# Optimization experiments

Measured on AMD Instinct MI355X. Metric: run time of the kernel, lower is better.

## Reference

```python
import jax, jax.numpy as jnp
import numpy as np

B, C, H, W = 8, 512, 96, 96
C8 = C // 8


def conv1x1(x, w, b):
    # x: (B,Cin,H,W), w: (Cout,Cin), b: (Cout,)
    return jnp.einsum('bchw,oc->bohw', x, w) + b[None, :, None, None]


def setup_inputs() -> dict:
    key = jax.random.key(0)
    ks = jax.random.split(key, 12)
    s = 0.05
    return {
        'x_exmplar': jax.random.normal(ks[0], (B, C, H, W), jnp.float32),
        'x_query': jax.random.normal(ks[1], (B, C, H, W), jnp.float32),
        'Wq': jax.random.normal(ks[2], (C8, C), jnp.float32) * s,
        'bq': jax.random.normal(ks[3], (C8,), jnp.float32) * s,
        'Wk': jax.random.normal(ks[4], (C8, C), jnp.float32) * s,
        'bk': jax.random.normal(ks[5], (C8,), jnp.float32) * s,
        'Wv': jax.random.normal(ks[6], (C, C), jnp.float32) * s,
        'bv': jax.random.normal(ks[7], (C,), jnp.float32) * s,
        'Wqv': jax.random.normal(ks[8], (C, C), jnp.float32) * s,
        'bqv': jax.random.normal(ks[9], (C,), jnp.float32) * s,
        'gamma1': jax.random.normal(ks[10], (1,), jnp.float32) * 0.5,
        'gamma2': jax.random.normal(ks[11], (1,), jnp.float32) * 0.5,
    }


def reference(x_exmplar, x_query, Wq, bq, Wk, bk, Wv, bv, Wqv, bqv, gamma1, gamma2):
    Bq, Cq, Hh, Ww = x_query.shape
    q = conv1x1(x_query, Wq, bq)        # (B,C8,H,W)
    k = conv1x1(x_exmplar, Wk, bk)      # (B,C8,H,W)
    v = conv1x1(x_exmplar, Wv, bv)      # (B,C,H,W)
    qv = conv1x1(x_query, Wqv, bqv)     # (B,C,H,W)

    # Criss-cross energies. energy_H masks the self position (INF diag).
    eH = jnp.einsum('bchw,bcjw->bhwj', q, k)            # (B,H,W,H)
    eye = jnp.eye(Hh, dtype=bool)                        # (H,H)
    eH = jnp.where(eye[:, None, :], -jnp.inf, eH)        # mask h==j
    eW = jnp.einsum('bchw,bchj->bhwj', q, k)             # (B,H,W,W)

    att = jax.nn.softmax(jnp.concatenate([eH, eW], axis=3), axis=3)
    att_H, att_W = att[..., :Hh], att[..., Hh:]          # (B,H,W,H),(B,H,W,W)

    out_H = jnp.einsum('bcjw,bhwj->bchw', v, att_H)
    out_W = jnp.einsum('bchj,bhwj->bchw', v, att_W)
    qout_H = jnp.einsum('bcjw,bhwj->bchw', qv, att_H)
    qout_W = jnp.einsum('bchj,bhwj->bchw', qv, att_W)

    # Diagonal (LR/RL) terms. Note: torch.diagonal of the transposed map equals
    # the diagonal itself, so energy_RL == energy_LR (faithful to original).
    qd = jnp.diagonal(q, axis1=2, axis2=3)               # (B,C8,D)
    kd = jnp.diagonal(k, axis1=2, axis2=3)
    vd = jnp.diagonal(v, axis1=2, axis2=3)               # (B,C,D)
    qvd = jnp.diagonal(qv, axis1=2, axis2=3)
    e_LR = jnp.einsum('bci,bcj->bij', kd, qd)            # (B,D,D)

    # softmax over a size-1 trailing axis (as in the original): yields ones,
    # broadcast-added over the width dim.
    out_LR = jax.nn.softmax(jnp.einsum('bcd,bdj->bcj', vd, e_LR)[..., None], axis=3)
    out_RL = jax.nn.softmax(jnp.einsum('bcd,bdj->bcj', vd, e_LR)[..., None], axis=3)
    qout_LR = jax.nn.softmax(jnp.einsum('bcd,bdj->bcj', qvd, e_LR)[..., None], axis=3)
    qout_RL = jax.nn.softmax(jnp.einsum('bcd,bdj->bcj', qvd, e_LR)[..., None], axis=3)

    examplar_att = out_H + out_W + out_LR + out_RL       # (B,C,H,W) via broadcast
    query_att = qout_H + qout_W + qout_LR + qout_RL
    return (gamma1 * examplar_att + x_exmplar, gamma2 * query_att + x_query)
```

## Files before the change

kernel.cpp:

```cpp
#include <hip/hip_runtime.h>
#include <math.h>

#define C_   512
#define C8_  64
#define HH   96
#define WW   96
#define PP   9216
#define CP   4718592
#define C8P  589824
#define ATTN 1769472

typedef __attribute__((ext_vector_type(4))) float f32x4;
typedef __attribute__((ext_vector_type(8))) __bf16 bf16x8;
typedef __attribute__((ext_vector_type(8))) unsigned short ushort8;
typedef __attribute__((ext_vector_type(4))) unsigned short ushort4v;
typedef __attribute__((ext_vector_type(2))) unsigned short ushort2v;
typedef __attribute__((ext_vector_type(2))) float float2v;

__device__ __forceinline__ float bf2f(unsigned short u) {
    union { unsigned u; float f; } x; x.u = ((unsigned)u) << 16; return x.f;
}
__device__ __forceinline__ unsigned short f2bf(float f) {
    union { float f; unsigned u; } x; x.f = f;
    unsigned r = x.u + 0x7fffu + ((x.u >> 16) & 1u);
    return (unsigned short)(r >> 16);
}
__device__ __forceinline__ void gload16(const void* g, void* l) {
    __builtin_amdgcn_global_load_lds(
        (const __attribute__((address_space(1))) unsigned int*)g,
        (__attribute__((address_space(3))) unsigned int*)l, 16, 0, 0);
}

__global__ __launch_bounds__(256) void cast_w(
    const float* __restrict__ Wv, const float* __restrict__ Wqv,
    const float* __restrict__ Wq, const float* __restrict__ Wk,
    unsigned short* __restrict__ oV, unsigned short* __restrict__ oQV,
    unsigned short* __restrict__ oQ, unsigned short* __restrict__ oK)
{
    int y = blockIdx.y;
    int n = (y < 2) ? 262144 : 32768;
    const float* s = (y == 0) ? Wv : (y == 1) ? Wqv : (y == 2) ? Wq : Wk;
    unsigned short* d = (y == 0) ? oV : (y == 1) ? oQV : (y == 2) ? oQ : oK;
    int i = (blockIdx.x * 256 + threadIdx.x) * 4;
    if (i < n) {
        float4 v = *(const float4*)(s + i);
        ushort4v o = { f2bf(v.x), f2bf(v.y), f2bf(v.z), f2bf(v.w) };
        *(ushort4v*)(d + i) = o;
    }
}

__global__ __launch_bounds__(256) void cast_transpose_cp(
    const float* __restrict__ xq, const float* __restrict__ xe,
    unsigned short* __restrict__ xTq, unsigned short* __restrict__ xTe)
{
    int zz = blockIdx.z;
    int which = zz & 1;
    size_t b = zz >> 1;
    const float* xb = (which ? xe : xq) + b * (size_t)CP;
    unsigned short* xTb = (which ? xTe : xTq) + b * (size_t)CP;
    int p0 = blockIdx.x * 64, c0 = blockIdx.y * 64;

    __shared__ unsigned short T[64][65];
    int t = threadIdx.x;
    int pp = t & 31, cg = t >> 5;
#pragma unroll
    for (int i = 0; i < 8; ++i) {
        int c = cg + 8 * i;
        float2v v = *(const float2v*)(xb + (size_t)(c0 + c) * PP + p0 + pp * 2);
        T[c][pp * 2] = f2bf(v.x);
        T[c][pp * 2 + 1] = f2bf(v.y);
    }
    __syncthreads();
    int cp = t & 31;
#pragma unroll
    for (int i = 0; i < 8; ++i) {
        int e = t + 256 * i;
        int p = e >> 5;
        ushort2v o = { T[cp * 2][p], T[cp * 2 + 1][p] };
        *(ushort2v*)(xTb + (size_t)(p0 + p) * C_ + c0 + cp * 2) = o;
    }
}

__global__ __launch_bounds__(256) void gemm_qk(
    const unsigned short* __restrict__ Wqb, const unsigned short* __restrict__ Wkb,
    const unsigned short* __restrict__ xTq, const unsigned short* __restrict__ xTe,
    const float* __restrict__ bq, const float* __restrict__ bk,
    unsigned short* __restrict__ qout, unsigned short* __restrict__ kout)
{
    int sel = blockIdx.y;
    const unsigned short* A = sel ? Wkb : Wqb;
    const float* bias = sel ? bk : bq;
    int p0 = blockIdx.x * 128;
    size_t b = blockIdx.z;
    const unsigned short* Bb = (sel ? xTe : xTq) + b * (size_t)CP;
    unsigned short* outb = (sel ? kout : qout) + b * (size_t)C8P;

    __shared__ __align__(16) unsigned short Asm[64 * 32];
    __shared__ __align__(16) unsigned short Bsm[128 * 32];

    int tid = threadIdx.x;
    int lane = tid & 63, wid = tid >> 6;
    int wr = wid >> 1, wc = wid & 1;
    int l15 = lane & 15, l4 = lane >> 4;
    f32x4 acc[2][4] = {};

    for (int k0 = 0; k0 < 512; k0 += 32) {
        int c = tid;
        gload16(A + (size_t)(c >> 2) * 512 + k0 + (c & 3) * 8, Asm + c * 8);
        gload16(Bb + (size_t)(p0 + (c >> 2)) * 512 + k0 + (c & 3) * 8, Bsm + c * 8);
        int cb = tid + 256;
        gload16(Bb + (size_t)(p0 + (cb >> 2)) * 512 + k0 + (cb & 3) * 8, Bsm + cb * 8);
        __syncthreads();
        bf16x8 af[2], bfr[4];
#pragma unroll
        for (int m = 0; m < 2; ++m)
            af[m] = *(const bf16x8*)&Asm[(wr * 32 + m * 16 + l15) * 32 + l4 * 8];
#pragma unroll
        for (int n = 0; n < 4; ++n)
            bfr[n] = *(const bf16x8*)&Bsm[(wc * 64 + n * 16 + l15) * 32 + l4 * 8];
#pragma unroll
        for (int m = 0; m < 2; ++m)
#pragma unroll
            for (int n = 0; n < 4; ++n)
                acc[m][n] = __builtin_amdgcn_mfma_f32_16x16x32_bf16(af[m], bfr[n], acc[m][n], 0, 0, 0);
        __syncthreads();
    }
#pragma unroll
    for (int m = 0; m < 2; ++m)
#pragma unroll
        for (int n = 0; n < 4; ++n) {
            int pcol = p0 + wc * 64 + n * 16 + l15;
#pragma unroll
            for (int r = 0; r < 4; ++r) {
                int orow = wr * 32 + m * 16 + l4 * 4 + r;
                outb[(size_t)orow * PP + pcol] = f2bf(acc[m][n][r] + bias[orow]);
            }
        }
}

__global__ __launch_bounds__(256) void thw_b(
    const unsigned short* __restrict__ in, unsigned short* __restrict__ out)
{
    size_t m = blockIdx.x;
    const unsigned short* im = in + m * (size_t)PP;
    unsigned short* om = out + m * (size_t)PP;
    __shared__ unsigned short T[96][97];
    int t = threadIdx.x;
#pragma unroll
    for (int i = 0; i < 18; ++i) {
        int v = t + 256 * i;
        int r = v / 48, pp = v - r * 48;
        ushort2v u = *(const ushort2v*)(im + r * 96 + pp * 2);
        T[r][pp * 2] = u.x;
        T[r][pp * 2 + 1] = u.y;
    }
    __syncthreads();
#pragma unroll
    for (int i = 0; i < 18; ++i) {
        int v = t + 256 * i;
        int w = v / 48, hh = v - w * 48;
        ushort2v o = { T[hh * 2][w], T[hh * 2 + 1][w] };
        *(ushort2v*)(om + w * 96 + hh * 2) = o;
    }
}

__global__ __launch_bounds__(256) void scores_kernel(
    const unsigned short* __restrict__ qT, const unsigned short* __restrict__ kT,
    const unsigned short* __restrict__ q, const unsigned short* __restrict__ k,
    unsigned short* __restrict__ attb, float* __restrict__ rsum0, float* __restrict__ rsum1)
{
    int s = blockIdx.x;
    int ori = blockIdx.y;
    size_t b = blockIdx.z;
    const unsigned short* qs = (ori ? q : qT) + b * (size_t)C8P;
    const unsigned short* ks = (ori ? k : kT) + b * (size_t)C8P;
    unsigned short* ab = attb + b * (size_t)ATTN;
    float* rs = (ori ? rsum1 : rsum0) + b * (size_t)PP;

    __shared__ float Qs[64][97];
    __shared__ float Ks[64][97];
    int t = threadIdx.x;
    for (int v = t; v < 64 * 12; v += 256) {
        int c = v / 12, gg = v - c * 12;
        size_t gi = (size_t)c * PP + (size_t)s * 96 + gg * 8;
        ushort8 uq = *(const ushort8*)(qs + gi);
        ushort8 uk = *(const ushort8*)(ks + gi);
#pragma unroll
        for (int kk = 0; kk < 8; ++kk) {
            Qs[c][gg * 8 + kk] = bf2f(uq[kk]);
            Ks[c][gg * 8 + kk] = bf2f(uk[kk]);
        }
    }
    __syncthreads();
    int tx = t & 15, ty = t >> 4;
    float acc[6][6] = {};
    for (int c = 0; c < 64; ++c) {
        float qf[6], kf[6];
#pragma unroll
        for (int i = 0; i < 6; ++i) { qf[i] = Qs[c][ty + 16 * i]; kf[i] = Ks[c][tx + 16 * i]; }
#pragma unroll
        for (int i = 0; i < 6; ++i)
#pragma unroll
            for (int j = 0; j < 6; ++j) acc[i][j] = fmaf(qf[i], kf[j], acc[i][j]);
    }
#pragma unroll
    for (int i = 0; i < 6; ++i) {
        int m = ty + 16 * i;
        size_t row = ori ? ((size_t)s * 96 + m) : ((size_t)m * 96 + s);
        unsigned short* rowp = ab + row * 192 + (ori ? 96 : 0);
        float part = 0.0f;
#pragma unroll
        for (int j = 0; j < 6; ++j) {
            int jj = tx + 16 * j;
            float e = (!ori && jj == m) ? 0.0f : __expf(acc[i][j] - 20.0f);
            part += e;
            rowp[jj] = f2bf(e);
        }
#pragma unroll
        for (int off = 1; off < 16; off <<= 1) part += __shfl_xor(part, off);
        if (tx == 0) rs[row] = part;
    }
}

template<int ORI>
__global__ __launch_bounds__(512) void apply_mfma(
    const unsigned short* __restrict__ xT_e, const unsigned short* __restrict__ xT_q,
    unsigned short* __restrict__ yT_e, unsigned short* __restrict__ yT_q,
    const unsigned short* __restrict__ attb,
    const float* __restrict__ rsum0, const float* __restrict__ rsum1)
{
    int s = blockIdx.x;
    int path = blockIdx.y >> 1, ct = blockIdx.y & 1;
    int c0 = ct * 256;
    size_t b = blockIdx.z;
    const unsigned short* X = (path ? xT_q : xT_e) + b * (size_t)CP;
    unsigned short* Y = (path ? yT_q : yT_e) + b * (size_t)CP;
    const unsigned short* ab = attb + b * (size_t)ATTN;
    const float* r0 = rsum0 + b * (size_t)PP;
    const float* r1 = rsum1 + b * (size_t)PP;

    __shared__ __align__(16) unsigned short Att[96][104];
    __shared__ __align__(16) unsigned short Xs[256][104];

    int tid = threadIdx.x;
    for (int v = tid; v < 96 * 12; v += 512) {
        int r = v / 12, gg = v - r * 12;
        size_t base = ORI ? ((size_t)(s * 96 + r) * 192 + 96) : ((size_t)(r * 96 + s) * 192);
        *(ushort8*)&Att[r][gg * 8] = *(const ushort8*)(ab + base + gg * 8);
    }
    for (int v = tid; v < 96 * 32; v += 512) {
        int j = v >> 5, cc = v & 31;
        size_t pj = ORI ? ((size_t)s * 96 + j) : ((size_t)j * 96 + s);
        ushort8 u = *(const ushort8*)(X + pj * C_ + c0 + cc * 8);
        int js = j ^ ((cc & 3) << 3);
#pragma unroll
        for (int e = 0; e < 8; ++e) Xs[cc * 8 + e][js] = u[e];
    }
    __syncthreads();

    int lane = tid & 63, wid = tid >> 6;
    int wm = wid >> 2, wn = wid & 3;
    int l15 = lane & 15, l4 = lane >> 4;
    f32x4 acc[3][4] = {};
#pragma unroll
    for (int k = 0; k < 3; ++k) {
        bf16x8 a[3], xx[4];
#pragma unroll
        for (int mi = 0; mi < 3; ++mi)
            a[mi] = *(const bf16x8*)&Att[wm * 48 + mi * 16 + l15][k * 32 + l4 * 8];
#pragma unroll
        for (int ni = 0; ni < 4; ++ni) {
            int row = wn * 64 + ni * 16 + l15;
            int gsw = (k * 4 + l4) ^ ((row >> 3) & 3);
            xx[ni] = *(const bf16x8*)&Xs[row][gsw * 8];
        }
#pragma unroll
        for (int mi = 0; mi < 3; ++mi)
#pragma unroll
            for (int ni = 0; ni < 4; ++ni)
                acc[mi][ni] = __builtin_amdgcn_mfma_f32_16x16x32_bf16(a[mi], xx[ni], acc[mi][ni], 0, 0, 0);
    }

#pragma unroll
    for (int mi = 0; mi < 3; ++mi) {
#pragma unroll
        for (int r = 0; r < 4; ++r) {
            int mrow = wm * 48 + mi * 16 + l4 * 4 + r;
            size_t p = ORI ? ((size_t)s * 96 + mrow) : ((size_t)mrow * 96 + s);
            float rinv = 0.0f;
            if (ORI) rinv = 1.0f / (r0[p] + r1[p]);
            size_t base = p * C_ + c0;
#pragma unroll
            for (int ni = 0; ni < 4; ++ni) {
                size_t idx = base + wn * 64 + ni * 16 + l15;
                if (ORI == 0) {
                    Y[idx] = f2bf(acc[mi][ni][r]);
                } else {
                    float tot = bf2f(Y[idx]) + acc[mi][ni][r];
                    Y[idx] = f2bf(tot * rinv);
                }
            }
        }
    }
}

__global__ __launch_bounds__(512) void gemm_out(
    const unsigned short* __restrict__ Wvb, const unsigned short* __restrict__ Wqvb,
    const unsigned short* __restrict__ yT_e, const unsigned short* __restrict__ yT_q,
    const float* __restrict__ bv, const float* __restrict__ bqv,
    const float* __restrict__ xe, const float* __restrict__ xq,
    const float* __restrict__ g1, const float* __restrict__ g2,
    float* __restrict__ o0, float* __restrict__ o1)
{
    int yy = blockIdx.y;
    int path = yy >> 2, ot = yy & 3;
    const unsigned short* A = path ? Wqvb : Wvb;
    const float* bias = path ? bqv : bv;
    int p0 = blockIdx.x * 128;
    int o0r = ot * 128;
    size_t b = blockIdx.z;
    const unsigned short* Bb = (path ? yT_q : yT_e) + b * (size_t)CP;
    const float* xb = (path ? xq : xe) + b * (size_t)CP;
    float* ob = (path ? o1 : o0) + b * (size_t)CP;
    float gam = (path ? g2 : g1)[0];

    __shared__ __align__(16) unsigned short Asm[2][128 * 64];
    __shared__ __align__(16) unsigned short Bsm[2][128 * 64];

    int tid = threadIdx.x;
    int lane = tid & 63, wid = tid >> 6;
    int wr = wid >> 2, wc = wid & 3;
    int l15 = lane & 15, l4 = lane >> 4;
    f32x4 acc[4][2] = {};

#pragma unroll
    for (int i = 0; i < 2; ++i) {
        int ch = tid + i * 512;
        int row = ch >> 3, slot = ch & 7;
        int gs = slot ^ (row & 7);
        gload16(A + (size_t)(o0r + row) * 512 + gs * 8, Asm[0] + ch * 8);
        gload16(Bb + (size_t)(p0 + row) * 512 + gs * 8, Bsm[0] + ch * 8);
    }
    __syncthreads();

#pragma unroll
    for (int k = 0; k < 8; ++k) {
        int cur = k & 1;
        if (k < 7) {
            int k0n = (k + 1) * 64;
            int nxt = cur ^ 1;
#pragma unroll
            for (int i = 0; i < 2; ++i) {
                int ch = tid + i * 512;
                int row = ch >> 3, slot = ch & 7;
                int gs = slot ^ (row & 7);
                gload16(A + (size_t)(o0r + row) * 512 + k0n + gs * 8, Asm[nxt] + ch * 8);
                gload16(Bb + (size_t)(p0 + row) * 512 + k0n + gs * 8, Bsm[nxt] + ch * 8);
            }
        }
#pragma unroll
        for (int ks = 0; ks < 2; ++ks) {
            bf16x8 af[4], bfr[2];
#pragma unroll
            for (int m = 0; m < 4; ++m) {
                int row = wr * 64 + m * 16 + l15;
                int sl = (ks * 4 + l4) ^ (row & 7);
                af[m] = *(const bf16x8*)&Asm[cur][row * 64 + sl * 8];
            }
#pragma unroll
            for (int n = 0; n < 2; ++n) {
                int row = wc * 32 + n * 16 + l15;
                int sl = (ks * 4 + l4) ^ (row & 7);
                bfr[n] = *(const bf16x8*)&Bsm[cur][row * 64 + sl * 8];
            }
#pragma unroll
            for (int m = 0; m < 4; ++m)
#pragma unroll
                for (int n = 0; n < 2; ++n)
                    acc[m][n] = __builtin_amdgcn_mfma_f32_16x16x32_bf16(af[m], bfr[n], acc[m][n], 0, 0, 0);
        }
        __syncthreads();
    }

#pragma unroll
    for (int m = 0; m < 4; ++m)
#pragma unroll
        for (int n = 0; n < 2; ++n) {
            int pcol = p0 + wc * 32 + n * 16 + l15;
#pragma unroll
            for (int r = 0; r < 4; ++r) {
                int orow = o0r + wr * 64 + m * 16 + l4 * 4 + r;
                size_t idx = (size_t)orow * PP + pcol;
                float val = acc[m][n][r] + bias[orow];
                ob[idx] = gam * (val + 2.0f) + xb[idx];
            }
        }
}

extern "C" void kernel_launch(void* const* d_in, const int* in_sizes, int n_in,
                              void* d_out, int out_size, void* d_ws, size_t ws_size,
                              hipStream_t stream)
{
    const float* x_ex = (const float*)d_in[0];
    const float* x_q  = (const float*)d_in[1];
    const float* Wq   = (const float*)d_in[2];
    const float* bq   = (const float*)d_in[3];
    const float* Wk   = (const float*)d_in[4];
    const float* bk   = (const float*)d_in[5];
    const float* Wv   = (const float*)d_in[6];
    const float* bv   = (const float*)d_in[7];
    const float* Wqv  = (const float*)d_in[8];
    const float* bqv  = (const float*)d_in[9];
    const float* g1   = (const float*)d_in[10];
    const float* g2   = (const float*)d_in[11];
    float* out0 = (float*)d_out;
    float* out1 = out0 + (size_t)8 * CP;

    unsigned short* hp = (unsigned short*)d_ws;
    unsigned short* Wvb  = hp; hp += 262144;
    unsigned short* Wqvb = hp; hp += 262144;
    unsigned short* Wqb  = hp; hp += 32768;
    unsigned short* Wkb  = hp; hp += 32768;
    size_t head = (size_t)(hp - (unsigned short*)d_ws) * 2;

    size_t perB = 4ull * CP + (size_t)ATTN + 4ull * C8P + 4ull * PP;
    int g = 8;
    while (g > 1 && head + (size_t)g * perB * 2 > ws_size) g >>= 1;

    unsigned short* p = hp;
    unsigned short* xT_e = p; p += (size_t)g * CP;
    unsigned short* xT_q = p; p += (size_t)g * CP;
    unsigned short* yT_e = p; p += (size_t)g * CP;
    unsigned short* yT_q = p; p += (size_t)g * CP;
    unsigned short* attb = p; p += (size_t)g * ATTN;
    unsigned short* qb   = p; p += (size_t)g * C8P;
    unsigned short* kb   = p; p += (size_t)g * C8P;
    unsigned short* qTb  = p; p += (size_t)g * C8P;
    unsigned short* kTb  = p; p += (size_t)g * C8P;
    float* rsum0 = (float*)p; p += (size_t)g * PP * 2;
    float* rsum1 = (float*)p; p += (size_t)g * PP * 2;

    cast_w<<<dim3(256, 4), 256, 0, stream>>>(Wv, Wqv, Wq, Wk, Wvb, Wqvb, Wqb, Wkb);

    for (int b0 = 0; b0 < 8; b0 += g) {
        const float* xe = x_ex + (size_t)b0 * CP;
        const float* xq = x_q  + (size_t)b0 * CP;
        float* o0 = out0 + (size_t)b0 * CP;
        float* o1 = out1 + (size_t)b0 * CP;

        cast_transpose_cp<<<dim3(144, 8, 2 * g), 256, 0, stream>>>(xq, xe, xT_q, xT_e);
        gemm_qk<<<dim3(72, 2, g), 256, 0, stream>>>(Wqb, Wkb, xT_q, xT_e, bq, bk, qb, kb);
        thw_b<<<dim3(2 * g * 64), 256, 0, stream>>>(qb, qTb);
        scores_kernel<<<dim3(96, 2, g), 256, 0, stream>>>(qTb, kTb, qb, kb, attb, rsum0, rsum1);
        apply_mfma<0><<<dim3(96, 4, g), 512, 0, stream>>>(xT_e, xT_q, yT_e, yT_q, attb, rsum0, rsum1);
        apply_mfma<1><<<dim3(96, 4, g), 512, 0, stream>>>(xT_e, xT_q, yT_e, yT_q, attb, rsum0, rsum1);
        gemm_out<<<dim3(72, 8, g), 512, 0, stream>>>(Wvb, Wqvb, yT_e, yT_q, bv, bqv,
                                                     xe, xq, g1, g2, o0, o1);
    }
}
```

Measured before the change: 583.6 us.

## Double-buffer GEMM LDS loads with explicit vmcnt waits in qk and output GEMMs

Both the q/k projection GEMM and the output value GEMM now issue the global-to-LDS loads for the next K-tile two stages ahead into alternating shared buffers. They wait with a partial s_waitcnt vmcnt instead of a full __syncthreads drain. The aim is to overlap global load latency with MFMA work, where previously each K-step fully stalled on its loads. The hand-counted vmcnt values depend on the exact number of outstanding load instructions per stage, so a compiler change that splits or merges loads could break correctness. The qk kernel also doubles its LDS use.

```diff
diff --git a/kernel.cpp b/kernel.cpp
--- a/kernel.cpp
+++ b/kernel.cpp
@@ -95,8 +95,8 @@
     const unsigned short* Bb = (sel ? xTe : xTq) + b * (size_t)CP;
     unsigned short* outb = (sel ? kout : qout) + b * (size_t)C8P;
 
-    __shared__ __align__(16) unsigned short Asm[64 * 32];
-    __shared__ __align__(16) unsigned short Bsm[128 * 32];
+    __shared__ __align__(16) unsigned short Asm[2][64 * 32];
+    __shared__ __align__(16) unsigned short Bsm[2][128 * 32];
 
     int tid = threadIdx.x;
     int lane = tid & 63, wid = tid >> 6;
@@ -104,27 +104,43 @@
     int l15 = lane & 15, l4 = lane >> 4;
     f32x4 acc[2][4] = {};
 
-    for (int k0 = 0; k0 < 512; k0 += 32) {
-        int c = tid;
-        gload16(A + (size_t)(c >> 2) * 512 + k0 + (c & 3) * 8, Asm + c * 8);
-        gload16(Bb + (size_t)(p0 + (c >> 2)) * 512 + k0 + (c & 3) * 8, Bsm + c * 8);
-        int cb = tid + 256;
-        gload16(Bb + (size_t)(p0 + (cb >> 2)) * 512 + k0 + (cb & 3) * 8, Bsm + cb * 8);
-        __syncthreads();
+#define QK_STAGE(KT, BUF)                                                              \
+    {                                                                                  \
+        int k0s = (KT) * 32;                                                           \
+        int c = tid;                                                                   \
+        gload16(A + (size_t)(c >> 2) * 512 + k0s + (c & 3) * 8, Asm[BUF] + c * 8);     \
+        gload16(Bb + (size_t)(p0 + (c >> 2)) * 512 + k0s + (c & 3) * 8, Bsm[BUF] + c * 8); \
+        int cb = tid + 256;                                                            \
+        gload16(Bb + (size_t)(p0 + (cb >> 2)) * 512 + k0s + (cb & 3) * 8, Bsm[BUF] + cb * 8); \
+    }
+
+    QK_STAGE(0, 0);
+    QK_STAGE(1, 1);
+
+#pragma unroll
+    for (int k = 0; k < 16; ++k) {
+        int cur = k & 1;
+        if (k < 15) asm volatile("s_waitcnt vmcnt(3)" ::: "memory");
+        else        asm volatile("s_waitcnt vmcnt(0)" ::: "memory");
+        __builtin_amdgcn_s_barrier();
         bf16x8 af[2], bfr[4];
 #pragma unroll
         for (int m = 0; m < 2; ++m)
-            af[m] = *(const bf16x8*)&Asm[(wr * 32 + m * 16 + l15) * 32 + l4 * 8];
+            af[m] = *(const bf16x8*)&Asm[cur][(wr * 32 + m * 16 + l15) * 32 + l4 * 8];
 #pragma unroll
         for (int n = 0; n < 4; ++n)
-            bfr[n] = *(const bf16x8*)&Bsm[(wc * 64 + n * 16 + l15) * 32 + l4 * 8];
+            bfr[n] = *(const bf16x8*)&Bsm[cur][(wc * 64 + n * 16 + l15) * 32 + l4 * 8];
 #pragma unroll
         for (int m = 0; m < 2; ++m)
 #pragma unroll
             for (int n = 0; n < 4; ++n)
                 acc[m][n] = __builtin_amdgcn_mfma_f32_16x16x32_bf16(af[m], bfr[n], acc[m][n], 0, 0, 0);
-        __syncthreads();
-    }
+        asm volatile("" ::: "memory");
+        __builtin_amdgcn_s_barrier();
+        if (k < 14) QK_STAGE(k + 2, cur);
+    }
+#undef QK_STAGE
+
 #pragma unroll
     for (int m = 0; m < 2; ++m)
 #pragma unroll
@@ -333,31 +349,28 @@
     int l15 = lane & 15, l4 = lane >> 4;
     f32x4 acc[4][2] = {};
 
-#pragma unroll
-    for (int i = 0; i < 2; ++i) {
-        int ch = tid + i * 512;
-        int row = ch >> 3, slot = ch & 7;
-        int gs = slot ^ (row & 7);
-        gload16(A + (size_t)(o0r + row) * 512 + gs * 8, Asm[0] + ch * 8);
-        gload16(Bb + (size_t)(p0 + row) * 512 + gs * 8, Bsm[0] + ch * 8);
-    }
-    __syncthreads();
+#define GO_STAGE(KT, BUF)                                                                  \
+    {                                                                                      \
+        int k0s = (KT) * 64;                                                               \
+        _Pragma("unroll")                                                                  \
+        for (int i = 0; i < 2; ++i) {                                                      \
+            int ch = tid + i * 512;                                                        \
+            int row = ch >> 3, slot = ch & 7;                                              \
+            int gs = slot ^ (row & 7);                                                     \
+            gload16(A + (size_t)(o0r + row) * 512 + k0s + gs * 8, Asm[BUF] + ch * 8);      \
+            gload16(Bb + (size_t)(p0 + row) * 512 + k0s + gs * 8, Bsm[BUF] + ch * 8);      \
+        }                                                                                  \
+    }
+
+    GO_STAGE(0, 0);
+    GO_STAGE(1, 1);
 
 #pragma unroll
     for (int k = 0; k < 8; ++k) {
         int cur = k & 1;
-        if (k < 7) {
-            int k0n = (k + 1) * 64;
-            int nxt = cur ^ 1;
-#pragma unroll
-            for (int i = 0; i < 2; ++i) {
-                int ch = tid + i * 512;
-                int row = ch >> 3, slot = ch & 7;
-                int gs = slot ^ (row & 7);
-                gload16(A + (size_t)(o0r + row) * 512 + k0n + gs * 8, Asm[nxt] + ch * 8);
-                gload16(Bb + (size_t)(p0 + row) * 512 + k0n + gs * 8, Bsm[nxt] + ch * 8);
-            }
-        }
+        if (k < 7) asm volatile("s_waitcnt vmcnt(4)" ::: "memory");
+        else       asm volatile("s_waitcnt vmcnt(0)" ::: "memory");
+        __builtin_amdgcn_s_barrier();
 #pragma unroll
         for (int ks = 0; ks < 2; ++ks) {
             bf16x8 af[4], bfr[2];
@@ -379,8 +392,11 @@
                 for (int n = 0; n < 2; ++n)
                     acc[m][n] = __builtin_amdgcn_mfma_f32_16x16x32_bf16(af[m], bfr[n], acc[m][n], 0, 0, 0);
         }
-        __syncthreads();
-    }
+        asm volatile("" ::: "memory");
+        __builtin_amdgcn_s_barrier();
+        if (k < 6) GO_STAGE(k + 2, cur);
+    }
+#undef GO_STAGE
 
 #pragma unroll
     for (int m = 0; m < 4; ++m)
```

Result: no change. 573.9 us (-1.7%).
